# Kernel optimization log

Measured on AMD Instinct MI355X. Metric: run time of the kernel, lower is better.

The kernel has to match this reference:

```python
import jax, jax.numpy as jnp
import numpy as np

N, M, F, B = 100000, 12, 64, 41  # atoms, max neighbors, atom feat dim, bond feat dim
EPS = 1e-5


def setup_inputs() -> dict:
    key = jax.random.key(0)
    ks = jax.random.split(key, 8)
    neighbor_indices = jax.random.randint(ks[0], (N, M), 0, N, dtype=jnp.int32)
    atom_features = jax.random.normal(ks[1], (N, F), dtype=jnp.float32)
    bond_features = jax.random.normal(ks[2], (N, M, B), dtype=jnp.float32)
    W = jax.random.normal(ks[3], (2 * F + B, 2 * F), dtype=jnp.float32) * 0.05
    b = jnp.zeros((2 * F,), dtype=jnp.float32)
    bn1_scale = 1.0 + 0.02 * jax.random.normal(ks[4], (2 * F,), dtype=jnp.float32)
    bn1_offset = 0.02 * jax.random.normal(ks[5], (2 * F,), dtype=jnp.float32)
    bn2_scale = 1.0 + 0.02 * jax.random.normal(ks[6], (F,), dtype=jnp.float32)
    bn2_offset = 0.02 * jax.random.normal(ks[7], (F,), dtype=jnp.float32)
    return {"neighbor_indices": neighbor_indices, "atom_features": atom_features,
            "bond_features": bond_features, "W": W, "b": b,
            "bn1_scale": bn1_scale, "bn1_offset": bn1_offset,
            "bn2_scale": bn2_scale, "bn2_offset": bn2_offset}


def batchnorm(x, scale, offset):
    # haiku BatchNorm, training mode: batch stats over all axes but channel (last)
    mean = jnp.mean(x, axis=0, keepdims=True)
    var = jnp.mean(jnp.square(x), axis=0, keepdims=True) - jnp.square(mean)
    inv = scale * jax.lax.rsqrt(var + EPS)
    return (x - mean) * inv + offset


def reference(neighbor_indices, atom_features, bond_features, W, b,
              bn1_scale, bn1_offset, bn2_scale, bn2_offset):
    n = atom_features.shape[0]
    nbr_feats = atom_features[neighbor_indices]  # (N, M, F) gather
    self_feats = jnp.broadcast_to(atom_features[:, None, :], (n, M, F))
    total = jnp.concatenate([self_feats, nbr_feats, bond_features], axis=2)  # (N, M, 2F+B)
    gated = total @ W + b  # (N, M, 2F)
    gated = batchnorm(gated.reshape(-1, 2 * F), bn1_scale, bn1_offset).reshape(n, M, 2 * F)
    nbr_filter, nbr_core = jnp.split(gated, 2, axis=2)
    summed = jnp.sum(jax.nn.sigmoid(nbr_filter) * jax.nn.softplus(nbr_core), axis=1)  # (N, F)
    summed = batchnorm(summed, bn2_scale, bn2_offset)
    return jax.nn.softplus(atom_features + summed)
```

## Files before the change

### kernel.cpp

```cpp
#include <hip/hip_runtime.h>
#include <hip/hip_bf16.h>
#include <math.h>


#define NATOMS  100000
#define MNBR    12
#define FDIM    64
#define BDIM    41
#define C2F     128
#define EPSBN   1e-5f
#define NBLK    2048
#define GROUPS  (NATOMS/4)
#define AR      136
#define PR      72

typedef __attribute__((ext_vector_type(8))) short  short8;
typedef __attribute__((ext_vector_type(4))) float  f32x4;

__device__ __forceinline__ float softplusf(float x) {
    return fmaxf(x, 0.f) + __logf(1.f + __expf(-fabsf(x)));
}
__device__ __forceinline__ float sigmoidf(float x) {
    return 1.f / (1.f + __expf(-x));
}
__device__ __forceinline__ unsigned short f2bf(float f) {
    unsigned int x = __builtin_bit_cast(unsigned int, f);
    unsigned int r = (x + 0x7fff + ((x >> 16) & 1)) >> 16;
    return (unsigned short)r;
}
__device__ __forceinline__ unsigned int pkbf(float a, float b) {
    unsigned short lo = __builtin_bit_cast(unsigned short, __float2bfloat16(a));
    unsigned short hi = __builtin_bit_cast(unsigned short, __float2bfloat16(b));
    return (unsigned)lo | ((unsigned)hi << 16);
}
__device__ __forceinline__ float bflo(unsigned int u) {
    return __builtin_bit_cast(float, u << 16);
}
__device__ __forceinline__ float bfhi(unsigned int u) {
    return __builtin_bit_cast(float, u & 0xffff0000u);
}
__device__ __forceinline__ float bf2f(unsigned short u) {
    return __builtin_bit_cast(float, ((unsigned int)u) << 16);
}

__global__ __launch_bounds__(256) void k_pack(
    const float* __restrict__ W,
    unsigned short* __restrict__ Wsn, unsigned short* __restrict__ Wpk)
{
    const int t0 = blockIdx.x*256 + threadIdx.x;
    for (int idx = t0; idx < 8*2*64*8; idx += gridDim.x*256) {
        int e = idx & 7, lane = (idx >> 3) & 63, ks = (idx >> 9) & 1, n = idx >> 10;
        int k   = ks*32 + (lane >> 4)*8 + e;
        int col = n*16 + (lane & 15);
        Wsn[idx] = f2bf(W[k*C2F + col]);
    }
    for (int idx = t0; idx < 8*4*64*8; idx += gridDim.x*256) {
        int e = idx & 7, lane = (idx >> 3) & 63, ks = (idx >> 9) & 3, n = idx >> 11;
        int k   = ks*32 + (lane >> 4)*8 + e;
        int col = n*16 + (lane & 15);
        float v = (k < 105) ? W[(64 + k)*C2F + col] : 0.f;
        Wpk[idx] = f2bf(v);
    }
}

__global__ __launch_bounds__(256, 4) void k_proj(
    const float* __restrict__ atomF, const unsigned short* __restrict__ Wsn,
    unsigned short* __restrict__ PselfBf, unsigned short* __restrict__ atomBf)
{
    __shared__ __align__(16) unsigned short A[64*PR];
    const int tid = threadIdx.x, w = tid >> 6, lane = tid & 63;
    const int g = lane >> 4, x = lane & 15;
    short8 B0[2], B1[2];
    #pragma unroll
    for (int ks = 0; ks < 2; ++ks) {
        B0[ks] = *(const short8*)(Wsn + ((w*2 + ks)*64 + lane)*8);
        B1[ks] = *(const short8*)(Wsn + (((w+4)*2 + ks)*64 + lane)*8);
    }
    for (int a0 = blockIdx.x*64; a0 < NATOMS; a0 += gridDim.x*64) {
        __syncthreads();
        #pragma unroll
        for (int it = 0; it < 4; ++it) {
            int idx = it*256 + tid;
            int p = idx >> 4, c = idx & 15;
            int i = a0 + p;
            float4 v = make_float4(0.f, 0.f, 0.f, 0.f);
            if (i < NATOMS) v = *(const float4*)(atomF + (size_t)i*FDIM + 4*c);
            uint2 u; u.x = pkbf(v.x, v.y); u.y = pkbf(v.z, v.w);
            *(uint2*)(A + p*PR + 4*c) = u;
            if (i < NATOMS) *(uint2*)(atomBf + (size_t)i*FDIM + 4*c) = u;
        }
        __syncthreads();
        f32x4 z = {0.f, 0.f, 0.f, 0.f};
        f32x4 acc[4][2];
        #pragma unroll
        for (int m = 0; m < 4; ++m) { acc[m][0] = z; acc[m][1] = z; }
        #pragma unroll
        for (int ks = 0; ks < 2; ++ks) {
            #pragma unroll
            for (int m = 0; m < 4; ++m) {
                short8 a = *(const short8*)(A + (m*16 + x)*PR + ks*32 + g*8);
                acc[m][0] = __builtin_amdgcn_mfma_f32_16x16x32_bf16(a, B0[ks], acc[m][0], 0, 0, 0);
                acc[m][1] = __builtin_amdgcn_mfma_f32_16x16x32_bf16(a, B1[ks], acc[m][1], 0, 0, 0);
            }
        }
        #pragma unroll
        for (int m = 0; m < 4; ++m) {
            int i = a0 + m*16 + g*4;
            #pragma unroll
            for (int rg = 0; rg < 4; ++rg) {
                if (i + rg < NATOMS) {
                    PselfBf[(size_t)(i+rg)*C2F + w*16 + x]     = f2bf(acc[m][0][rg]);
                    PselfBf[(size_t)(i+rg)*C2F + (w+4)*16 + x] = f2bf(acc[m][1][rg]);
                }
            }
        }
    }
}

__global__ __launch_bounds__(512, 4) void k_gemm(
    const int* __restrict__ nbr, const unsigned short* __restrict__ atomBf,
    const float* __restrict__ bond, const unsigned short* __restrict__ Wpk,
    const unsigned short* __restrict__ PselfBf,
    uint2* __restrict__ gated, float* __restrict__ partial1)
{
    __shared__ __align__(16) unsigned short A[2][48*AR];
    const int tid = threadIdx.x, w = tid >> 6, lane = tid & 63;
    const int g = lane >> 4, x = lane & 15;
    const int ch = w*16 + x;
    short8 B[4];
    #pragma unroll
    for (int ks = 0; ks < 4; ++ks)
        B[ks] = *(const short8*)(Wpk + ((w*4 + ks)*64 + lane)*8);
    for (int idx = tid; idx < 2*48*AR/2; idx += 512) ((unsigned int*)A)[idx] = 0u;

    uint2 st[3];
    int rN[3] = {0,0,0};
    int rM[3] = {0,0,0};
    float s = 0.f, q = 0.f;

#define LOAD_NBR(GRP, R)                                                      \
    {   const int base_ = (GRP)*4;                                            \
        _Pragma("unroll")                                                     \
        for (int it = 0; it < 3; ++it) {                                      \
            int idx = it*512 + tid;                                           \
            int p = idx >> 5, c = idx & 31;                                   \
            if (c < 16) R[it] = nbr[base_*MNBR + p];                          \
        } }

#define GATHER(GRP, R)                                                        \
    {   const int base_ = (GRP)*4;                                            \
        _Pragma("unroll")                                                     \
        for (int it = 0; it < 3; ++it) {                                      \
            int idx = it*512 + tid;                                           \
            int p = idx >> 5, c = idx & 31;                                   \
            if (c < 16) {                                                     \
                st[it] = *(const uint2*)(atomBf + ((size_t)R[it] << 6) + 4*c);\
            } else if (c < 27) {                                              \
                int cc = c - 16;                                              \
                int pa = p/12;                                                \
                const float* bp = bond + (size_t)(base_ + pa)*(MNBR*BDIM)     \
                                       + (p - pa*12)*BDIM + 4*cc;             \
                float b0 = bp[0], b1 = 0.f, b2 = 0.f, b3 = 0.f;               \
                if (cc < 10) { b1 = bp[1]; b2 = bp[2]; b3 = bp[3]; }          \
                st[it].x = pkbf(b0, b1); st[it].y = pkbf(b2, b3);             \
            }                                                                 \
        } }

#define WRITEA(BUF)                                                           \
    {   _Pragma("unroll")                                                     \
        for (int it = 0; it < 3; ++it) {                                      \
            int idx = it*512 + tid;                                           \
            int p = idx >> 5, c = idx & 31;                                   \
            if (c < 16)      *(uint2*)(&A[BUF][p*AR + 4*c]) = st[it];         \
            else if (c < 27) *(uint2*)(&A[BUF][p*AR + 64 + 4*(c-16)]) = st[it]; \
        } }

    const int S = gridDim.x;
    int grp = blockIdx.x;
    int cur = 0;
    if (grp < GROUPS) {
        LOAD_NBR(grp, rN);
        GATHER(grp, rN);
        WRITEA(0);
        if (grp + S < GROUPS) LOAD_NBR(grp + S, rN);
    }
    for (; grp < GROUPS; grp += S) {
        const int nxt = grp + S;
        __syncthreads();
        if (nxt < GROUPS) GATHER(nxt, rN);
        if (nxt + S < GROUPS) LOAD_NBR(nxt + S, rM);
        f32x4 z = {0.f, 0.f, 0.f, 0.f};
        f32x4 acc[3];
        acc[0] = z; acc[1] = z; acc[2] = z;
        #pragma unroll
        for (int ks = 0; ks < 4; ++ks) {
            #pragma unroll
            for (int m = 0; m < 3; ++m) {
                short8 a = *(const short8*)(&A[cur][(m*16 + x)*AR + ks*32 + g*8]);
                acc[m] = __builtin_amdgcn_mfma_f32_16x16x32_bf16(a, B[ks], acc[m], 0, 0, 0);
            }
        }
        const int base = grp*4;
        #pragma unroll
        for (int m = 0; m < 3; ++m) {
            int ia = base + (m*16 + g*4)/12;
            float ps = bf2f(PselfBf[(size_t)ia*C2F + ch]);
            float v0 = acc[m][0] + ps, v1 = acc[m][1] + ps;
            float v2 = acc[m][2] + ps, v3 = acc[m][3] + ps;
            s += (v0 + v1) + (v2 + v3);
            q = fmaf(v0, v0, q); q = fmaf(v1, v1, q);
            q = fmaf(v2, v2, q); q = fmaf(v3, v3, q);
            uint2 pk;
            pk.x = pkbf(v0, v1); pk.y = pkbf(v2, v3);
            gated[(((size_t)grp*3 + m)*8 + w)*64 + lane] = pk;
        }
        if (nxt < GROUPS) WRITEA(cur ^ 1);
        #pragma unroll
        for (int it = 0; it < 3; ++it) rN[it] = rM[it];
        cur ^= 1;
    }
#undef LOAD_NBR
#undef GATHER
#undef WRITEA
    s += __shfl_xor(s, 16); s += __shfl_xor(s, 32);
    q += __shfl_xor(q, 16); q += __shfl_xor(q, 32);
    if (g == 0) {
        float* pb = partial1 + blockIdx.x*256;
        pb[ch]       = s;
        pb[128 + ch] = q;
    }
}

__global__ __launch_bounds__(256) void k_red(
    const float* __restrict__ in, float* __restrict__ outp, int width)
{
    const int b = blockIdx.x;
    for (int c = threadIdx.x; c < width; c += 256) {
        float s = 0.f;
        #pragma unroll 4
        for (int k = 0; k < 16; ++k) s += in[(size_t)(b*16 + k)*width + c];
        outp[(size_t)b*width + c] = s;
    }
}

__global__ __launch_bounds__(1024) void k_bn1_finalize(
    const float* __restrict__ red1, const float* __restrict__ scale,
    const float* __restrict__ offset, float* __restrict__ prm1)
{
    __shared__ float redS[1024], redQ[1024];
    const int tid = threadIdx.x, c = tid & 127, h = tid >> 7;
    float S = 0.f, Q = 0.f;
    for (int blk = h; blk < 128; blk += 8) {
        S += red1[blk*256 + c];
        Q += red1[blk*256 + 128 + c];
    }
    redS[tid] = S; redQ[tid] = Q;
    __syncthreads();
    if (tid < 128) {
        float Sa = 0.f, Qa = 0.f;
        #pragma unroll
        for (int hh = 0; hh < 8; ++hh) { Sa += redS[hh*128 + c]; Qa += redQ[hh*128 + c]; }
        const float invn = 1.f / (float)(NATOMS * MNBR);
        float mean = Sa * invn;
        float var  = Qa * invn - mean*mean;
        float inv  = scale[c] * rsqrtf(var + EPSBN);
        prm1[c]       = inv;
        prm1[128 + c] = offset[c] - mean*inv;
    }
}

__global__ __launch_bounds__(256, 8) void k_apply(
    const uint2* __restrict__ gated, const float* __restrict__ prm1,
    float* __restrict__ summed, float* __restrict__ partial2)
{
    __shared__ float Y[12*66];
    __shared__ float red[256];
    const int tid = threadIdx.x, w = tid >> 6, lane = tid & 63;
    const int g = lane >> 4, x = lane & 15;
    const int ch0 = w*16 + x;
    const float iv0 = prm1[ch0],      of0 = prm1[C2F + ch0];
    const float iv1 = prm1[64 + ch0], of1 = prm1[C2F + 64 + ch0];
    float s2 = 0.f, q2 = 0.f;

    for (int grp = blockIdx.x; grp < GROUPS; grp += gridDim.x) {
        __syncthreads();
        #pragma unroll
        for (int m = 0; m < 3; ++m) {
            const uint2* gb = gated + ((size_t)grp*3 + m)*8*64;
            uint2 uF = gb[w*64 + lane];
            uint2 uC = gb[(w+4)*64 + lane];
            float y00 = bflo(uF.x)*iv0 + of0, y01 = bfhi(uF.x)*iv0 + of0;
            float y02 = bflo(uF.y)*iv0 + of0, y03 = bfhi(uF.y)*iv0 + of0;
            float y10 = bflo(uC.x)*iv1 + of1, y11 = bfhi(uC.x)*iv1 + of1;
            float y12 = bflo(uC.y)*iv1 + of1, y13 = bfhi(uC.y)*iv1 + of1;
            float sY = sigmoidf(y00)*softplusf(y10) + sigmoidf(y01)*softplusf(y11)
                     + sigmoidf(y02)*softplusf(y12) + sigmoidf(y03)*softplusf(y13);
            Y[(m*4 + g)*66 + ch0] = sY;
        }
        __syncthreads();
        float sv = Y[(3*w)*66 + lane] + Y[(3*w + 1)*66 + lane] + Y[(3*w + 2)*66 + lane];
        summed[(size_t)(grp*4 + w)*FDIM + lane] = sv;
        s2 += sv; q2 = fmaf(sv, sv, q2);
    }
    red[tid] = s2; __syncthreads();
    if (tid < 64) partial2[blockIdx.x*128 + tid]
        = red[tid] + red[tid+64] + red[tid+128] + red[tid+192];
    __syncthreads();
    red[tid] = q2; __syncthreads();
    if (tid < 64) partial2[blockIdx.x*128 + 64 + tid]
        = red[tid] + red[tid+64] + red[tid+128] + red[tid+192];
}

__global__ __launch_bounds__(1024) void k_bn2_finalize(
    const float* __restrict__ red2, const float* __restrict__ scale,
    const float* __restrict__ offset, float* __restrict__ prm2)
{
    __shared__ float redS[1024], redQ[1024];
    const int tid = threadIdx.x, f = tid & 63, h = tid >> 6;
    float S = 0.f, Q = 0.f;
    for (int blk = h; blk < 128; blk += 16) {
        S += red2[blk*128 + f];
        Q += red2[blk*128 + 64 + f];
    }
    redS[tid] = S; redQ[tid] = Q;
    __syncthreads();
    if (tid < 64) {
        float Sa = 0.f, Qa = 0.f;
        #pragma unroll
        for (int hh = 0; hh < 16; ++hh) { Sa += redS[hh*64 + f]; Qa += redQ[hh*64 + f]; }
        const float invn = 1.f / (float)NATOMS;
        float mean = Sa * invn;
        float var  = Qa * invn - mean*mean;
        float inv  = scale[f] * rsqrtf(var + EPSBN);
        prm2[f]      = inv;
        prm2[64 + f] = offset[f] - mean*inv;
    }
}

__global__ __launch_bounds__(256) void k_final(
    const float* __restrict__ atomF, const float* __restrict__ summed,
    const float* __restrict__ prm2, float* __restrict__ out)
{
    __shared__ float iv[64], of[64];
    if (threadIdx.x < 64) {
        iv[threadIdx.x] = prm2[threadIdx.x];
        of[threadIdx.x] = prm2[64 + threadIdx.x];
    }
    __syncthreads();
    const int total4 = NATOMS*FDIM/4;
    for (int t = blockIdx.x*blockDim.x + threadIdx.x; t < total4;
         t += gridDim.x*blockDim.x) {
        float4 a = ((const float4*)atomF)[t];
        float4 s = ((const float4*)summed)[t];
        int fb = (t*4) & 63;
        float4 r;
        r.x = softplusf(a.x + s.x*iv[fb]   + of[fb]);
        r.y = softplusf(a.y + s.y*iv[fb+1] + of[fb+1]);
        r.z = softplusf(a.z + s.z*iv[fb+2] + of[fb+2]);
        r.w = softplusf(a.w + s.w*iv[fb+3] + of[fb+3]);
        ((float4*)out)[t] = r;
    }
}

extern "C" void kernel_launch(void* const* d_in, const int* in_sizes, int n_in,
                              void* d_out, int out_size, void* d_ws, size_t ws_size,
                              hipStream_t stream)
{
    const int*   nbr   = (const int*)  d_in[0];
    const float* atomF = (const float*)d_in[1];
    const float* bond  = (const float*)d_in[2];
    const float* W     = (const float*)d_in[3];
    const float* s1    = (const float*)d_in[5];
    const float* o1    = (const float*)d_in[6];
    const float* s2    = (const float*)d_in[7];
    const float* o2    = (const float*)d_in[8];
    float* out = (float*)d_out;

    uint2* gated        = (uint2*)d_ws;
    unsigned short* PselfBf = (unsigned short*)(gated + (size_t)GROUPS*3*8*64);
    unsigned short* atomBf  = PselfBf + (size_t)NATOMS*C2F;
    float* summed   = (float*)(atomBf + (size_t)NATOMS*FDIM);
    float* partial1 = summed   + (size_t)NATOMS*FDIM;
    float* partial2 = partial1 + (size_t)NBLK*256;
    float* red1     = partial2 + (size_t)NBLK*128;
    float* red2     = red1     + 128*256;
    float* prm1     = red2     + 128*128;
    float* prm2     = prm1     + 256;
    unsigned short* Wsn = (unsigned short*)(prm2 + 128);
    unsigned short* Wpk = Wsn + 8192;

    hipLaunchKernelGGL(k_pack,         dim3(64),   dim3(256),  0, stream, W, Wsn, Wpk);
    hipLaunchKernelGGL(k_proj,         dim3(782),  dim3(256),  0, stream,
                       atomF, Wsn, PselfBf, atomBf);
    hipLaunchKernelGGL(k_gemm,         dim3(NBLK), dim3(512),  0, stream,
                       nbr, atomBf, bond, Wpk, PselfBf, gated, partial1);
    hipLaunchKernelGGL(k_red,          dim3(128),  dim3(256),  0, stream, partial1, red1, 256);
    hipLaunchKernelGGL(k_bn1_finalize, dim3(1),    dim3(1024), 0, stream, red1, s1, o1, prm1);
    hipLaunchKernelGGL(k_apply,        dim3(NBLK), dim3(256),  0, stream,
                       gated, prm1, summed, partial2);
    hipLaunchKernelGGL(k_red,          dim3(128),  dim3(256),  0, stream, partial2, red2, 128);
    hipLaunchKernelGGL(k_bn2_finalize, dim3(1),    dim3(1024), 0, stream, red2, s2, o2, prm2);
    hipLaunchKernelGGL(k_final,        dim3(2048), dim3(256),  0, stream, atomF, summed, prm2, out);
}
```

Measured before the change: 399.5 us.

## Make each wave process whole neighbor groups with register-resident A fragments

```diff
diff --git a/kernel.cpp b/kernel.cpp
--- a/kernel.cpp
+++ b/kernel.cpp
@@ -10,8 +10,8 @@
 #define C2F     128
 #define EPSBN   1e-5f
 #define NBLK    2048
+#define NWAVES  (NBLK*4)
 #define GROUPS  (NATOMS/4)
-#define AR      136
 #define PR      72
 
 typedef __attribute__((ext_vector_type(8))) short  short8;
@@ -117,128 +117,106 @@
     }
 }
 
-__global__ __launch_bounds__(512, 4) void k_gemm(
+__global__ __launch_bounds__(256, 3) void k_gemm(
     const int* __restrict__ nbr, const unsigned short* __restrict__ atomBf,
     const float* __restrict__ bond, const unsigned short* __restrict__ Wpk,
     const unsigned short* __restrict__ PselfBf,
     uint2* __restrict__ gated, float* __restrict__ partial1)
 {
-    __shared__ __align__(16) unsigned short A[2][48*AR];
+    __shared__ __align__(16) unsigned short Wl[16384];
     const int tid = threadIdx.x, w = tid >> 6, lane = tid & 63;
     const int g = lane >> 4, x = lane & 15;
-    const int ch = w*16 + x;
-    short8 B[4];
-    #pragma unroll
-    for (int ks = 0; ks < 4; ++ks)
-        B[ks] = *(const short8*)(Wpk + ((w*4 + ks)*64 + lane)*8);
-    for (int idx = tid; idx < 2*48*AR/2; idx += 512) ((unsigned int*)A)[idx] = 0u;
-
-    uint2 st[3];
-    int rN[3] = {0,0,0};
-    int rM[3] = {0,0,0};
-    float s = 0.f, q = 0.f;
-
-#define LOAD_NBR(GRP, R)                                                      \
-    {   const int base_ = (GRP)*4;                                            \
-        _Pragma("unroll")                                                     \
-        for (int it = 0; it < 3; ++it) {                                      \
-            int idx = it*512 + tid;                                           \
-            int p = idx >> 5, c = idx & 31;                                   \
-            if (c < 16) R[it] = nbr[base_*MNBR + p];                          \
-        } }
-
-#define GATHER(GRP, R)                                                        \
-    {   const int base_ = (GRP)*4;                                            \
-        _Pragma("unroll")                                                     \
-        for (int it = 0; it < 3; ++it) {                                      \
-            int idx = it*512 + tid;                                           \
-            int p = idx >> 5, c = idx & 31;                                   \
-            if (c < 16) {                                                     \
-                st[it] = *(const uint2*)(atomBf + ((size_t)R[it] << 6) + 4*c);\
-            } else if (c < 27) {                                              \
-                int cc = c - 16;                                              \
-                int pa = p/12;                                                \
-                const float* bp = bond + (size_t)(base_ + pa)*(MNBR*BDIM)     \
-                                       + (p - pa*12)*BDIM + 4*cc;             \
-                float b0 = bp[0], b1 = 0.f, b2 = 0.f, b3 = 0.f;               \
-                if (cc < 10) { b1 = bp[1]; b2 = bp[2]; b3 = bp[3]; }          \
-                st[it].x = pkbf(b0, b1); st[it].y = pkbf(b2, b3);             \
-            }                                                                 \
-        } }
-
-#define WRITEA(BUF)                                                           \
-    {   _Pragma("unroll")                                                     \
-        for (int it = 0; it < 3; ++it) {                                      \
-            int idx = it*512 + tid;                                           \
-            int p = idx >> 5, c = idx & 31;                                   \
-            if (c < 16)      *(uint2*)(&A[BUF][p*AR + 4*c]) = st[it];         \
-            else if (c < 27) *(uint2*)(&A[BUF][p*AR + 64 + 4*(c-16)]) = st[it]; \
-        } }
-
-    const int S = gridDim.x;
-    int grp = blockIdx.x;
-    int cur = 0;
-    if (grp < GROUPS) {
-        LOAD_NBR(grp, rN);
-        GATHER(grp, rN);
-        WRITEA(0);
-        if (grp + S < GROUPS) LOAD_NBR(grp + S, rN);
-    }
-    for (; grp < GROUPS; grp += S) {
-        const int nxt = grp + S;
-        __syncthreads();
-        if (nxt < GROUPS) GATHER(nxt, rN);
-        if (nxt + S < GROUPS) LOAD_NBR(nxt + S, rM);
-        f32x4 z = {0.f, 0.f, 0.f, 0.f};
-        f32x4 acc[3];
-        acc[0] = z; acc[1] = z; acc[2] = z;
-        #pragma unroll
-        for (int ks = 0; ks < 4; ++ks) {
+    for (int i = tid; i < 8192; i += 256)
+        ((unsigned int*)Wl)[i] = ((const unsigned int*)Wpk)[i];
+    __syncthreads();
+
+    float s[8] = {0,0,0,0,0,0,0,0};
+    float q[8] = {0,0,0,0,0,0,0,0};
+    const int wid = blockIdx.x*4 + w;
+    const int NW  = gridDim.x*4;
+
+    for (int grp = wid; grp < GROUPS; grp += NW) {
+        const int base4 = grp*4;
+        uint4 A[3][4];
+        int   ia[3];
+        #pragma unroll
+        for (int m = 0; m < 3; ++m) {
+            const int p = m*16 + x;
+            const int r = nbr[grp*48 + p];
+            const unsigned short* ab = atomBf + ((size_t)r << 6);
+            A[m][0] = *(const uint4*)(ab +      g*8);
+            A[m][1] = *(const uint4*)(ab + 32 + g*8);
+            const float* bp = bond + ((size_t)grp*48 + p)*BDIM;
+            {
+                float b0 = bp[g*8+0], b1 = bp[g*8+1], b2 = bp[g*8+2], b3 = bp[g*8+3];
+                float b4 = bp[g*8+4], b5 = bp[g*8+5], b6 = bp[g*8+6], b7 = bp[g*8+7];
+                A[m][2].x = pkbf(b0,b1); A[m][2].y = pkbf(b2,b3);
+                A[m][2].z = pkbf(b4,b5); A[m][2].w = pkbf(b6,b7);
+            }
+            uint4 a3 = {0u,0u,0u,0u};
+            if (g == 0) {
+                float c0 = bp[32], c1 = bp[33], c2 = bp[34], c3 = bp[35];
+                float c4 = bp[36], c5 = bp[37], c6 = bp[38], c7 = bp[39];
+                a3.x = pkbf(c0,c1); a3.y = pkbf(c2,c3);
+                a3.z = pkbf(c4,c5); a3.w = pkbf(c6,c7);
+            } else if (g == 1) {
+                a3.x = pkbf(bp[40], 0.f);
+            }
+            A[m][3] = a3;
+            ia[m] = base4 + (m*16 + g*4)/12;
+        }
+        #pragma unroll
+        for (int n = 0; n < 8; ++n) {
+            short8 B0 = *(const short8*)(Wl + ((n*4 + 0)*64 + lane)*8);
+            short8 B1 = *(const short8*)(Wl + ((n*4 + 1)*64 + lane)*8);
+            short8 B2 = *(const short8*)(Wl + ((n*4 + 2)*64 + lane)*8);
+            short8 B3 = *(const short8*)(Wl + ((n*4 + 3)*64 + lane)*8);
+            const int ch = n*16 + x;
             #pragma unroll
             for (int m = 0; m < 3; ++m) {
-                short8 a = *(const short8*)(&A[cur][(m*16 + x)*AR + ks*32 + g*8]);
-                acc[m] = __builtin_amdgcn_mfma_f32_16x16x32_bf16(a, B[ks], acc[m], 0, 0, 0);
-            }
-        }
-        const int base = grp*4;
-        #pragma unroll
-        for (int m = 0; m < 3; ++m) {
-            int ia = base + (m*16 + g*4)/12;
-            float ps = bf2f(PselfBf[(size_t)ia*C2F + ch]);
-            float v0 = acc[m][0] + ps, v1 = acc[m][1] + ps;
-            float v2 = acc[m][2] + ps, v3 = acc[m][3] + ps;
-            s += (v0 + v1) + (v2 + v3);
-            q = fmaf(v0, v0, q); q = fmaf(v1, v1, q);
-            q = fmaf(v2, v2, q); q = fmaf(v3, v3, q);
-            uint2 pk;
-            pk.x = pkbf(v0, v1); pk.y = pkbf(v2, v3);
-            gated[(((size_t)grp*3 + m)*8 + w)*64 + lane] = pk;
-        }
-        if (nxt < GROUPS) WRITEA(cur ^ 1);
-        #pragma unroll
-        for (int it = 0; it < 3; ++it) rN[it] = rM[it];
-        cur ^= 1;
-    }
-#undef LOAD_NBR
-#undef GATHER
-#undef WRITEA
-    s += __shfl_xor(s, 16); s += __shfl_xor(s, 32);
-    q += __shfl_xor(q, 16); q += __shfl_xor(q, 32);
+                f32x4 acc = {0.f, 0.f, 0.f, 0.f};
+                acc = __builtin_amdgcn_mfma_f32_16x16x32_bf16(
+                          __builtin_bit_cast(short8, A[m][0]), B0, acc, 0, 0, 0);
+                acc = __builtin_amdgcn_mfma_f32_16x16x32_bf16(
+                          __builtin_bit_cast(short8, A[m][1]), B1, acc, 0, 0, 0);
+                acc = __builtin_amdgcn_mfma_f32_16x16x32_bf16(
+                          __builtin_bit_cast(short8, A[m][2]), B2, acc, 0, 0, 0);
+                acc = __builtin_amdgcn_mfma_f32_16x16x32_bf16(
+                          __builtin_bit_cast(short8, A[m][3]), B3, acc, 0, 0, 0);
+                float ps = bf2f(PselfBf[(size_t)ia[m]*C2F + ch]);
+                float v0 = acc[0] + ps, v1 = acc[1] + ps;
+                float v2 = acc[2] + ps, v3 = acc[3] + ps;
+                s[n] += (v0 + v1) + (v2 + v3);
+                q[n] = fmaf(v0, v0, q[n]); q[n] = fmaf(v1, v1, q[n]);
+                q[n] = fmaf(v2, v2, q[n]); q[n] = fmaf(v3, v3, q[n]);
+                uint2 pk;
+                pk.x = pkbf(v0, v1); pk.y = pkbf(v2, v3);
+                gated[(((size_t)grp*3 + m)*8 + n)*64 + lane] = pk;
+            }
+        }
+    }
+    #pragma unroll
+    for (int n = 0; n < 8; ++n) {
+        s[n] += __shfl_xor(s[n], 16); s[n] += __shfl_xor(s[n], 32);
+        q[n] += __shfl_xor(q[n], 16); q[n] += __shfl_xor(q[n], 32);
+    }
     if (g == 0) {
-        float* pb = partial1 + blockIdx.x*256;
-        pb[ch]       = s;
-        pb[128 + ch] = q;
+        float* pb = partial1 + (size_t)wid*256;
+        #pragma unroll
+        for (int n = 0; n < 8; ++n) {
+            pb[n*16 + x]       = s[n];
+            pb[128 + n*16 + x] = q[n];
+        }
     }
 }
 
 __global__ __launch_bounds__(256) void k_red(
-    const float* __restrict__ in, float* __restrict__ outp, int width)
+    const float* __restrict__ in, float* __restrict__ outp, int width, int per)
 {
     const int b = blockIdx.x;
     for (int c = threadIdx.x; c < width; c += 256) {
         float s = 0.f;
-        #pragma unroll 4
-        for (int k = 0; k < 16; ++k) s += in[(size_t)(b*16 + k)*width + c];
+        for (int k = 0; k < per; ++k) s += in[(size_t)(b*per + k)*width + c];
         outp[(size_t)b*width + c] = s;
     }
 }
@@ -381,7 +359,7 @@
     unsigned short* atomBf  = PselfBf + (size_t)NATOMS*C2F;
     float* summed   = (float*)(atomBf + (size_t)NATOMS*FDIM);
     float* partial1 = summed   + (size_t)NATOMS*FDIM;
-    float* partial2 = partial1 + (size_t)NBLK*256;
+    float* partial2 = partial1 + (size_t)NWAVES*256;
     float* red1     = partial2 + (size_t)NBLK*128;
     float* red2     = red1     + 128*256;
     float* prm1     = red2     + 128*128;
@@ -392,13 +370,15 @@
     hipLaunchKernelGGL(k_pack,         dim3(64),   dim3(256),  0, stream, W, Wsn, Wpk);
     hipLaunchKernelGGL(k_proj,         dim3(782),  dim3(256),  0, stream,
                        atomF, Wsn, PselfBf, atomBf);
-    hipLaunchKernelGGL(k_gemm,         dim3(NBLK), dim3(512),  0, stream,
+    hipLaunchKernelGGL(k_gemm,         dim3(NBLK), dim3(256),  0, stream,
                        nbr, atomBf, bond, Wpk, PselfBf, gated, partial1);
-    hipLaunchKernelGGL(k_red,          dim3(128),  dim3(256),  0, stream, partial1, red1, 256);
+    hipLaunchKernelGGL(k_red,          dim3(128),  dim3(256),  0, stream,
+                       partial1, red1, 256, NWAVES/128);
     hipLaunchKernelGGL(k_bn1_finalize, dim3(1),    dim3(1024), 0, stream, red1, s1, o1, prm1);
     hipLaunchKernelGGL(k_apply,        dim3(NBLK), dim3(256),  0, stream,
                        gated, prm1, summed, partial2);
-    hipLaunchKernelGGL(k_red,          dim3(128),  dim3(256),  0, stream, partial2, red2, 128);
+    hipLaunchKernelGGL(k_red,          dim3(128),  dim3(256),  0, stream,
+                       partial2, red2, 128, NBLK/128);
     hipLaunchKernelGGL(k_bn2_finalize, dim3(1),    dim3(1024), 0, stream, red2, s2, o2, prm2);
     hipLaunchKernelGGL(k_final,        dim3(2048), dim3(256),  0, stream, atomF, summed, prm2, out);
 }
```

Result: slower. 828.9 us (+107.5%).
